# Kernel tuning notes

Measured on AMD Instinct MI355X. Metric: run time of the kernel, lower is better.

Reference implementation:

```python
import jax, jax.numpy as jnp
import numpy as np
from jax import lax


def _depthwise3x3(x, filt2d):
    # x: [B, C, H, W]; filt2d: [3, 3]. Depthwise conv with padding=1.
    C = x.shape[1]
    kern = jnp.broadcast_to(filt2d, (C, 1, 3, 3)).astype(x.dtype)  # OIHW, groups=C
    return lax.conv_general_dilated(
        x, kern, window_strides=(1, 1), padding=((1, 1), (1, 1)),
        feature_group_count=C,
        dimension_numbers=("NCHW", "OIHW", "NCHW"))


def setup_inputs() -> dict:
    key = jax.random.key(0)
    k_x, k_w0, k_b0, k_w1, k_u = jax.random.split(key, 5)
    B, C, H, W, HID = 4, 16, 512, 512, 128
    x = jax.random.normal(k_x, (B, C, H, W), dtype=jnp.float32)
    # torch nn.Linear layout: weight [out, in]
    w0 = jax.random.normal(k_w0, (HID, 3 * C), dtype=jnp.float32) * 0.1
    b0 = jax.random.normal(k_b0, (HID,), dtype=jnp.float32) * 0.1
    # original zero-inits fc1; use small random values for a non-trivial baseline
    w1 = jax.random.normal(k_w1, (C, HID), dtype=jnp.float32) * 0.1
    rand_u = jax.random.uniform(k_u, (B, 1, H, W), dtype=jnp.float32)
    return {"x": x, "w0": w0, "b0": b0, "w1": w1, "rand_u": rand_u}


def reference(x, w0, b0, w1, rand_u):
    sobel_x = jnp.array([[-1.0, 0.0, 1.0],
                         [-2.0, 0.0, 2.0],
                         [-1.0, 0.0, 1.0]], dtype=x.dtype)
    sobel_y = sobel_x.T
    grad_x = _depthwise3x3(x, sobel_x)
    grad_y = _depthwise3x3(x, sobel_y)
    y = jnp.concatenate([x, grad_x, grad_y], axis=1)          # [B, 3C, H, W]
    y = jnp.transpose(y, (0, 2, 3, 1))                        # [B, H, W, 3C]
    h = jax.nn.relu(jnp.einsum('bhwc,oc->bhwo', y, w0) + b0)  # [B, H, W, HID]
    update = jnp.einsum('bhwo,ko->bhwk', h, w1)               # [B, H, W, C]
    update = jnp.transpose(update, (0, 3, 1, 2))              # [B, C, H, W]
    mask = (rand_u > 0.5).astype(x.dtype)                     # [B, 1, H, W]
    return x + update * mask
```

## Files before the change

### kernel.cpp

```cpp
#include <hip/hip_runtime.h>
#include <cstddef>

#define BATCH 4
#define CH    16
#define HH    512
#define WW    512
#define HID   128
#define K3    48
#define YSTR  72
#define HSTR  136
#define XSTR  17

typedef __bf16 bf16x8 __attribute__((ext_vector_type(8)));
typedef __bf16 bf16x4 __attribute__((ext_vector_type(4)));
typedef float  f32x4  __attribute__((ext_vector_type(4)));

static __device__ __forceinline__ f32x4 mfma16(bf16x8 a, bf16x8 b, f32x4 c) {
    return __builtin_amdgcn_mfma_f32_16x16x32_bf16(a, b, c, 0, 0, 0);
}

__global__ __launch_bounds__(256, 3)
void ca_mfma5(const float* __restrict__ x, const float* __restrict__ w0,
              const float* __restrict__ b0, const float* __restrict__ w1,
              const float* __restrict__ ru, float* __restrict__ out)
{
    __shared__ __align__(16) __bf16 sW0[2 * 8 * 64 * 8];
    __shared__ __align__(16) __bf16 sW1[4 * 64 * 8];
    __shared__ __align__(16) __bf16 sY[64 * YSTR];
    __shared__ __align__(16) __bf16 sH[64 * HSTR];
    __shared__ float sXC[64 * XSTR];
    __shared__ float sRU[WW];

    const int tid  = threadIdx.x;
    const int lane = tid & 63;
    const int wv   = tid >> 6;
    const int p    = lane & 15;
    const int q    = lane >> 4;

    const int orig = blockIdx.x;
    const int row  = ((orig & 7) << 8) | (orig >> 3);
    const int b    = row >> 9;
    const int i    = row & (HH - 1);

    const size_t plane = (size_t)HH * WW;
    const float* xb    = x + (size_t)b * CH * plane + (size_t)i * WW;
    const bool   up    = (i > 0), dn = (i < HH - 1);
    const int    px    = tid & 63;

    float LA[4][9], LB[4][9];

    auto issue_loads = [&](int s, float (&L)[4][9]) {
        const int j  = s * 64 + px;
        const bool lf = (j > 0), rt = (j < WW - 1);
        #pragma unroll
        for (int k = 0; k < 4; ++k) {
            const float* c0 = xb + (size_t)(4 * wv + k) * plane + j;
            L[k][0] = (up && lf) ? c0[-WW - 1] : 0.f;
            L[k][1] =  up        ? c0[-WW]     : 0.f;
            L[k][2] = (up && rt) ? c0[-WW + 1] : 0.f;
            L[k][3] =  lf        ? c0[-1]      : 0.f;
            L[k][4] =              c0[0];
            L[k][5] =  rt        ? c0[1]       : 0.f;
            L[k][6] = (dn && lf) ? c0[WW - 1]  : 0.f;
            L[k][7] =  dn        ? c0[WW]      : 0.f;
            L[k][8] = (dn && rt) ? c0[WW + 1]  : 0.f;
        }
    };

    issue_loads(0, LA);
    issue_loads(1, LB);

    for (int e = tid; e < 1024; e += 256) {
        const int ks = e >> 9, rem = e & 511;
        const int t = rem >> 6, ln = rem & 63;
        const int pp = ln & 15, qq = ln >> 4;
        const int o = 16 * t + pp;
        bf16x8 v;
        #pragma unroll
        for (int j = 0; j < 8; ++j) {
            const int k = 32 * ks + 8 * qq + j;
            float val;
            if (k < K3)       val = w0[o * K3 + k];
            else if (k == K3) val = b0[o];
            else              val = 0.f;
            v[j] = (__bf16)val;
        }
        *(bf16x8*)&sW0[e * 8] = v;
    }
    {
        const int e = tid;
        const int s = e >> 6, ln = e & 63;
        const int pp = ln & 15, qq = ln >> 4;
        bf16x8 v;
        #pragma unroll
        for (int j = 0; j < 8; ++j)
            v[j] = (__bf16)w1[pp * HID + 32 * s + 8 * qq + j];
        *(bf16x8*)&sW1[e * 8] = v;
    }
    for (int e = tid; e < WW; e += 256)
        sRU[e] = ru[(size_t)b * plane + (size_t)i * WW + e];
    if (tid < 64) {
        bf16x8 z0, z1;
        #pragma unroll
        for (int j = 0; j < 8; ++j) { z0[j] = (__bf16)0.f; z1[j] = (__bf16)0.f; }
        z0[0] = (__bf16)1.0f;
        *(bf16x8*)&sY[tid * YSTR + 48] = z0;
        *(bf16x8*)&sY[tid * YSTR + 56] = z1;
    }
    asm volatile("s_waitcnt lgkmcnt(0)");
    __builtin_amdgcn_s_barrier();

    auto seg_body = [&](int s, float (&L)[4][9]) {
        float fm[4], fgx[4], fgy[4];
        #pragma unroll
        for (int k = 0; k < 4; ++k) {
            fm[k]  = L[k][4];
            fgx[k] = (L[k][2] - L[k][0]) + 2.f * (L[k][5] - L[k][3]) + (L[k][8] - L[k][6]);
            fgy[k] = (L[k][6] - L[k][0]) + 2.f * (L[k][7] - L[k][1]) + (L[k][8] - L[k][2]);
        }
        if (s < 6) issue_loads(s + 2, L);
        __builtin_amdgcn_sched_barrier(0);

        __builtin_amdgcn_s_barrier();
        #pragma unroll
        for (int k = 0; k < 4; ++k) {
            const int ch = 4 * wv + k;
            sY[px * YSTR + ch]          = (__bf16)fm[k];
            sY[px * YSTR + CH + ch]     = (__bf16)fgx[k];
            sY[px * YSTR + 2 * CH + ch] = (__bf16)fgy[k];
            sXC[px * XSTR + ch]         = fm[k];
        }
        asm volatile("s_waitcnt lgkmcnt(0)");
        __builtin_amdgcn_s_barrier();

        const int pxg = 16 * wv + p;
        const bf16x8 yb0 = *(const bf16x8*)&sY[pxg * YSTR + 8 * q];
        const bf16x8 yb1 = *(const bf16x8*)&sY[pxg * YSTR + 32 + 8 * q];

        f32x4 acc[8];
        #pragma unroll
        for (int t = 0; t < 8; ++t) {
            const bf16x8 a0 = *(const bf16x8*)&sW0[((0 * 8 + t) * 64 + lane) * 8];
            const bf16x8 a1 = *(const bf16x8*)&sW0[((1 * 8 + t) * 64 + lane) * 8];
            acc[t] = f32x4{0.f, 0.f, 0.f, 0.f};
            acc[t] = mfma16(a0, yb0, acc[t]);
            acc[t] = mfma16(a1, yb1, acc[t]);
        }
        #pragma unroll
        for (int t = 0; t < 8; ++t) {
            bf16x4 hv;
            #pragma unroll
            for (int r = 0; r < 4; ++r)
                hv[r] = (__bf16)fmaxf(acc[t][r], 0.f);
            *(bf16x4*)&sH[pxg * HSTR + 16 * t + 4 * q] = hv;
        }
        f32x4 u = f32x4{0.f, 0.f, 0.f, 0.f};
        #pragma unroll
        for (int ss = 0; ss < 4; ++ss) {
            const bf16x8 hb = *(const bf16x8*)&sH[pxg * HSTR + 32 * ss + 8 * q];
            const bf16x8 aw = *(const bf16x8*)&sW1[(ss * 64 + lane) * 8];
            u = mfma16(aw, hb, u);
        }

        const int jg = s * 64 + pxg;
        const float rv = sRU[jg];
        const float m  = (rv > 0.5f) ? 1.f : 0.f;
        float* ob = out + (size_t)b * CH * plane + (size_t)i * WW + jg;
        #pragma unroll
        for (int r = 0; r < 4; ++r) {
            const int c = 4 * q + r;
            ob[(size_t)c * plane] = fmaf(u[r], m, sXC[pxg * XSTR + c]);
        }
    };

    for (int sp = 0; sp < 4; ++sp) {
        seg_body(2 * sp,     LA);
        seg_body(2 * sp + 1, LB);
    }
}

extern "C" void kernel_launch(void* const* d_in, const int* in_sizes, int n_in,
                              void* d_out, int out_size, void* d_ws, size_t ws_size,
                              hipStream_t stream) {
    const float* x  = (const float*)d_in[0];
    const float* w0 = (const float*)d_in[1];
    const float* b0 = (const float*)d_in[2];
    const float* w1 = (const float*)d_in[3];
    const float* ru = (const float*)d_in[4];
    float* out = (float*)d_out;

    dim3 grid(BATCH * HH);
    dim3 block(256);
    hipLaunchKernelGGL(ca_mfma5, grid, block, 0, stream, x, w0, b0, w1, ru, out);
}
```

Measured before the change: 203.2 us.

## Single-buffer stencil loads and keep W0 MFMA operands in registers

Drops the two-deep register double-buffer of the 3x3 stencil loads (LA/LB) for one buffer, with the next segment's loads issued after the LDS barrier. The W0 A-operand fragments are hoisted out of the segment loop into registers instead of being re-read from LDS every segment, and the MFMA and ReLU/store loops are fused so only one accumulator is live at a time. This cuts LDS traffic and register pressure from the second load buffer, but leaves less global-load latency hidden, since only one segment of loads is in flight.

```diff
diff --git a/kernel.cpp b/kernel.cpp
--- a/kernel.cpp
+++ b/kernel.cpp
@@ -20,7 +20,7 @@
 }
 
 __global__ __launch_bounds__(256, 3)
-void ca_mfma5(const float* __restrict__ x, const float* __restrict__ w0,
+void ca_mfma7(const float* __restrict__ x, const float* __restrict__ w0,
               const float* __restrict__ b0, const float* __restrict__ w1,
               const float* __restrict__ ru, float* __restrict__ out)
 {
@@ -47,9 +47,9 @@
     const bool   up    = (i > 0), dn = (i < HH - 1);
     const int    px    = tid & 63;
 
-    float LA[4][9], LB[4][9];
+    float L[4][9];
 
-    auto issue_loads = [&](int s, float (&L)[4][9]) {
+    auto issue_loads = [&](int s) {
         const int j  = s * 64 + px;
         const bool lf = (j > 0), rt = (j < WW - 1);
         #pragma unroll
@@ -67,8 +67,7 @@
         }
     };
 
-    issue_loads(0, LA);
-    issue_loads(1, LB);
+    issue_loads(0);
 
     for (int e = tid; e < 1024; e += 256) {
         const int ks = e >> 9, rem = e & 511;
@@ -110,7 +109,14 @@
     asm volatile("s_waitcnt lgkmcnt(0)");
     __builtin_amdgcn_s_barrier();
 
-    auto seg_body = [&](int s, float (&L)[4][9]) {
+    bf16x8 a0r[8], a1r[8];
+    #pragma unroll
+    for (int t = 0; t < 8; ++t) {
+        a0r[t] = *(const bf16x8*)&sW0[((0 * 8 + t) * 64 + lane) * 8];
+        a1r[t] = *(const bf16x8*)&sW0[((1 * 8 + t) * 64 + lane) * 8];
+    }
+
+    for (int s = 0; s < 8; ++s) {
         float fm[4], fgx[4], fgy[4];
         #pragma unroll
         for (int k = 0; k < 4; ++k) {
@@ -118,9 +124,6 @@
             fgx[k] = (L[k][2] - L[k][0]) + 2.f * (L[k][5] - L[k][3]) + (L[k][8] - L[k][6]);
             fgy[k] = (L[k][6] - L[k][0]) + 2.f * (L[k][7] - L[k][1]) + (L[k][8] - L[k][2]);
         }
-        if (s < 6) issue_loads(s + 2, L);
-        __builtin_amdgcn_sched_barrier(0);
-
         __builtin_amdgcn_s_barrier();
         #pragma unroll
         for (int k = 0; k < 4; ++k) {
@@ -133,25 +136,21 @@
         asm volatile("s_waitcnt lgkmcnt(0)");
         __builtin_amdgcn_s_barrier();
 
+        if (s < 7) issue_loads(s + 1);
+
         const int pxg = 16 * wv + p;
         const bf16x8 yb0 = *(const bf16x8*)&sY[pxg * YSTR + 8 * q];
         const bf16x8 yb1 = *(const bf16x8*)&sY[pxg * YSTR + 32 + 8 * q];
 
-        f32x4 acc[8];
         #pragma unroll
         for (int t = 0; t < 8; ++t) {
-            const bf16x8 a0 = *(const bf16x8*)&sW0[((0 * 8 + t) * 64 + lane) * 8];
-            const bf16x8 a1 = *(const bf16x8*)&sW0[((1 * 8 + t) * 64 + lane) * 8];
-            acc[t] = f32x4{0.f, 0.f, 0.f, 0.f};
-            acc[t] = mfma16(a0, yb0, acc[t]);
-            acc[t] = mfma16(a1, yb1, acc[t]);
-        }
-        #pragma unroll
-        for (int t = 0; t < 8; ++t) {
+            f32x4 acc = f32x4{0.f, 0.f, 0.f, 0.f};
+            acc = mfma16(a0r[t], yb0, acc);
+            acc = mfma16(a1r[t], yb1, acc);
             bf16x4 hv;
             #pragma unroll
             for (int r = 0; r < 4; ++r)
-                hv[r] = (__bf16)fmaxf(acc[t][r], 0.f);
+                hv[r] = (__bf16)fmaxf(acc[r], 0.f);
             *(bf16x4*)&sH[pxg * HSTR + 16 * t + 4 * q] = hv;
         }
         f32x4 u = f32x4{0.f, 0.f, 0.f, 0.f};
@@ -171,11 +170,6 @@
             const int c = 4 * q + r;
             ob[(size_t)c * plane] = fmaf(u[r], m, sXC[pxg * XSTR + c]);
         }
-    };
-
-    for (int sp = 0; sp < 4; ++sp) {
-        seg_body(2 * sp,     LA);
-        seg_body(2 * sp + 1, LB);
     }
 }
 
@@ -191,5 +185,5 @@
 
     dim3 grid(BATCH * HH);
     dim3 block(256);
-    hipLaunchKernelGGL(ca_mfma5, grid, block, 0, stream, x, w0, b0, w1, ru, out);
+    hipLaunchKernelGGL(ca_mfma7, grid, block, 0, stream, x, w0, b0, w1, ru, out);
 }
```

Measured after the change: 223.7 us. 1.1x slower.

## Vectorize LDS staging, keep first W0 fragment in registers, move prefetch after barrier

Applied to the files above, without the earlier changes.

Padding strides change so the per-pixel channel writes to sY and sXC become single 4-wide vector stores, and the sXC readback is one 16-byte load. The first half of the W0 MFMA operands is loaded once into registers instead of being re-read from LDS every segment. The next-segment global prefetch is moved after the LDS write barrier. The goals are fewer LDS instructions and less LDS traffic. The extra 32 VGPRs per thread may hurt occupancy under the 3-block launch bound, and the new strides may introduce bank conflicts.

```diff
diff --git a/kernel.cpp b/kernel.cpp
--- a/kernel.cpp
+++ b/kernel.cpp
@@ -7,9 +7,9 @@
 #define WW    512
 #define HID   128
 #define K3    48
-#define YSTR  72
+#define YSTR  68
 #define HSTR  136
-#define XSTR  17
+#define XSTR  20
 
 typedef __bf16 bf16x8 __attribute__((ext_vector_type(8)));
 typedef __bf16 bf16x4 __attribute__((ext_vector_type(4)));
@@ -20,7 +20,7 @@
 }
 
 __global__ __launch_bounds__(256, 3)
-void ca_mfma5(const float* __restrict__ x, const float* __restrict__ w0,
+void ca_mfma8(const float* __restrict__ x, const float* __restrict__ w0,
               const float* __restrict__ b0, const float* __restrict__ w1,
               const float* __restrict__ ru, float* __restrict__ out)
 {
@@ -28,7 +28,7 @@
     __shared__ __align__(16) __bf16 sW1[4 * 64 * 8];
     __shared__ __align__(16) __bf16 sY[64 * YSTR];
     __shared__ __align__(16) __bf16 sH[64 * HSTR];
-    __shared__ float sXC[64 * XSTR];
+    __shared__ __align__(16) float sXC[64 * XSTR];
     __shared__ float sRU[WW];
 
     const int tid  = threadIdx.x;
@@ -100,15 +100,22 @@
     for (int e = tid; e < WW; e += 256)
         sRU[e] = ru[(size_t)b * plane + (size_t)i * WW + e];
     if (tid < 64) {
-        bf16x8 z0, z1;
-        #pragma unroll
-        for (int j = 0; j < 8; ++j) { z0[j] = (__bf16)0.f; z1[j] = (__bf16)0.f; }
-        z0[0] = (__bf16)1.0f;
-        *(bf16x8*)&sY[tid * YSTR + 48] = z0;
-        *(bf16x8*)&sY[tid * YSTR + 56] = z1;
+        bf16x4 zb = {(__bf16)1.0f, (__bf16)0.f, (__bf16)0.f, (__bf16)0.f};
+        bf16x4 zz = {(__bf16)0.f, (__bf16)0.f, (__bf16)0.f, (__bf16)0.f};
+        *(bf16x4*)&sY[tid * YSTR + 48] = zb;
+        *(bf16x4*)&sY[tid * YSTR + 52] = zz;
+        *(bf16x4*)&sY[tid * YSTR + 56] = zz;
+        *(bf16x4*)&sY[tid * YSTR + 60] = zz;
     }
     asm volatile("s_waitcnt lgkmcnt(0)");
     __builtin_amdgcn_s_barrier();
+
+    bf16x8 a0r[8];
+    #pragma unroll
+    for (int t = 0; t < 8; ++t) {
+        a0r[t] = *(const bf16x8*)&sW0[((0 * 8 + t) * 64 + lane) * 8];
+        asm volatile("" : "+v"(a0r[t]));
+    }
 
     auto seg_body = [&](int s, float (&L)[4][9]) {
         float fm[4], fgx[4], fgy[4];
@@ -118,20 +125,21 @@
             fgx[k] = (L[k][2] - L[k][0]) + 2.f * (L[k][5] - L[k][3]) + (L[k][8] - L[k][6]);
             fgy[k] = (L[k][6] - L[k][0]) + 2.f * (L[k][7] - L[k][1]) + (L[k][8] - L[k][2]);
         }
-        if (s < 6) issue_loads(s + 2, L);
-        __builtin_amdgcn_sched_barrier(0);
-
         __builtin_amdgcn_s_barrier();
-        #pragma unroll
-        for (int k = 0; k < 4; ++k) {
-            const int ch = 4 * wv + k;
-            sY[px * YSTR + ch]          = (__bf16)fm[k];
-            sY[px * YSTR + CH + ch]     = (__bf16)fgx[k];
-            sY[px * YSTR + 2 * CH + ch] = (__bf16)fgy[k];
-            sXC[px * XSTR + ch]         = fm[k];
+        {
+            bf16x4 vm = {(__bf16)fm[0],  (__bf16)fm[1],  (__bf16)fm[2],  (__bf16)fm[3]};
+            bf16x4 vx = {(__bf16)fgx[0], (__bf16)fgx[1], (__bf16)fgx[2], (__bf16)fgx[3]};
+            bf16x4 vy = {(__bf16)fgy[0], (__bf16)fgy[1], (__bf16)fgy[2], (__bf16)fgy[3]};
+            *(bf16x4*)&sY[px * YSTR + 4 * wv]          = vm;
+            *(bf16x4*)&sY[px * YSTR + CH + 4 * wv]     = vx;
+            *(bf16x4*)&sY[px * YSTR + 2 * CH + 4 * wv] = vy;
+            f32x4 vc = {fm[0], fm[1], fm[2], fm[3]};
+            *(f32x4*)&sXC[px * XSTR + 4 * wv] = vc;
         }
         asm volatile("s_waitcnt lgkmcnt(0)");
         __builtin_amdgcn_s_barrier();
+
+        if (s < 6) issue_loads(s + 2, L);
 
         const int pxg = 16 * wv + p;
         const bf16x8 yb0 = *(const bf16x8*)&sY[pxg * YSTR + 8 * q];
@@ -140,11 +148,10 @@
         f32x4 acc[8];
         #pragma unroll
         for (int t = 0; t < 8; ++t) {
-            const bf16x8 a0 = *(const bf16x8*)&sW0[((0 * 8 + t) * 64 + lane) * 8];
             const bf16x8 a1 = *(const bf16x8*)&sW0[((1 * 8 + t) * 64 + lane) * 8];
             acc[t] = f32x4{0.f, 0.f, 0.f, 0.f};
-            acc[t] = mfma16(a0, yb0, acc[t]);
-            acc[t] = mfma16(a1, yb1, acc[t]);
+            acc[t] = mfma16(a0r[t], yb0, acc[t]);
+            acc[t] = mfma16(a1,     yb1, acc[t]);
         }
         #pragma unroll
         for (int t = 0; t < 8; ++t) {
@@ -165,11 +172,12 @@
         const int jg = s * 64 + pxg;
         const float rv = sRU[jg];
         const float m  = (rv > 0.5f) ? 1.f : 0.f;
+        const f32x4 xc = *(const f32x4*)&sXC[pxg * XSTR + 4 * q];
         float* ob = out + (size_t)b * CH * plane + (size_t)i * WW + jg;
         #pragma unroll
         for (int r = 0; r < 4; ++r) {
             const int c = 4 * q + r;
-            ob[(size_t)c * plane] = fmaf(u[r], m, sXC[pxg * XSTR + c]);
+            ob[(size_t)c * plane] = fmaf(u[r], m, xc[r]);
         }
     };
 
@@ -191,5 +199,5 @@
 
     dim3 grid(BATCH * HH);
     dim3 block(256);
-    hipLaunchKernelGGL(ca_mfma5, grid, block, 0, stream, x, w0, b0, w1, ru, out);
+    hipLaunchKernelGGL(ca_mfma8, grid, block, 0, stream, x, w0, b0, w1, ru, out);
 }
```

New measurement: 263.5 us. 29.7% more time.
